# Kernel optimization log

Measured on AMD Instinct MI355X. Metric: run time of the kernel, lower is better.

The kernel has to match this reference:

```python
import jax, jax.numpy as jnp
import numpy as np
import math

N_NODES = 100000
N_EDGES = 1600000
IN_C, HID_C, OUT_C = 512, 128, 64
N_LAYERS = 8
ALPHA = 0.1
THETA = 0.5


def setup_inputs() -> dict:
    key = jax.random.key(0)
    ks = jax.random.split(key, 6)
    x = jax.random.normal(ks[0], (N_NODES, IN_C), dtype=jnp.float32)
    edge_index = jax.random.randint(ks[1], (2, N_EDGES), 0, N_NODES, dtype=jnp.int32)
    edge_weight = jax.random.uniform(ks[2], (N_EDGES,), dtype=jnp.float32)
    # parameters (scaled for numerical sanity)
    W_enc = jax.random.normal(ks[3], (HID_C, IN_C), dtype=jnp.float32) * (1.0 / math.sqrt(IN_C))
    W_convs = jax.random.normal(ks[4], (N_LAYERS, HID_C, HID_C), dtype=jnp.float32) * (1.0 / math.sqrt(HID_C))
    W_dec = jax.random.normal(ks[5], (OUT_C, HID_C), dtype=jnp.float32) * (1.0 / math.sqrt(HID_C))
    return {"x": x, "edge_index": edge_index, "edge_weight": edge_weight,
            "W_enc": W_enc, "W_convs": W_convs, "W_dec": W_dec}


def reference(x, edge_index, edge_weight, W_enc, W_convs, W_dec):
    # eval mode: dropout is a no-op
    src, dst = edge_index[0], edge_index[1]
    h = x @ W_enc.T                      # [N, HID]
    x0 = h                               # initial residual
    for i in range(N_LAYERS):
        # sparse neighbor aggregation: agg[d] = sum_e w_e * h[src_e]
        msg = h[src] * edge_weight[:, None]                      # [E, HID]
        agg = jax.ops.segment_sum(msg, dst, num_segments=N_NODES)
        hh = (1.0 - ALPHA) * agg + ALPHA * x0                    # initial residual
        beta = math.log(THETA / (i + 1) + 1.0)                   # identity mapping weight
        h = jax.nn.relu((1.0 - beta) * hh + beta * (hh @ W_convs[i]))
    return h @ W_dec.T                   # [N, OUT]
```

## Files before the change

kernel.cpp:

```cpp
#include <hip/hip_runtime.h>
#include <math.h>

#define N_NODES 100000
#define N_EDGES 1600000
#define IN_C 512
#define HID_C 128
#define OUT_C 64
#define N_LAYERS 8

typedef short bf16x8 __attribute__((ext_vector_type(8)));
typedef float f32x4 __attribute__((ext_vector_type(4)));

static __device__ __forceinline__ ushort f2bf(float f) {
  uint u = __float_as_uint(f);
  u = (u + 0x7FFFu + ((u >> 16) & 1u)) >> 16;
  return (ushort)u;
}
static __device__ __forceinline__ float bflo(uint u) { return __uint_as_float(u << 16); }
static __device__ __forceinline__ float bfhi(uint u) { return __uint_as_float(u & 0xffff0000u); }

__global__ __launch_bounds__(256) void hist_kernel(const int* __restrict__ dst,
                                                   int* __restrict__ cnt) {
  int e = blockIdx.x * 256 + threadIdx.x;
  atomicAdd(&cnt[dst[e]], 1);
}

__global__ __launch_bounds__(256) void scan_block(const int* __restrict__ in,
                                                  int* __restrict__ out,
                                                  int* __restrict__ bsum, int n) {
  __shared__ int tsum[256];
  int t = threadIdx.x;
  int base = blockIdx.x * 1024 + t * 4;
  int v0 = (base + 0 < n) ? in[base + 0] : 0;
  int v1 = (base + 1 < n) ? in[base + 1] : 0;
  int v2 = (base + 2 < n) ? in[base + 2] : 0;
  int v3 = (base + 3 < n) ? in[base + 3] : 0;
  int s = v0 + v1 + v2 + v3;
  tsum[t] = s;
  __syncthreads();
  for (int off = 1; off < 256; off <<= 1) {
    int x = (t >= off) ? tsum[t - off] : 0;
    __syncthreads();
    tsum[t] += x;
    __syncthreads();
  }
  int excl = tsum[t] - s;
  int i0 = excl + v0, i1 = i0 + v1, i2 = i1 + v2, i3 = i2 + v3;
  if (base + 0 < n) out[base + 0] = i0;
  if (base + 1 < n) out[base + 1] = i1;
  if (base + 2 < n) out[base + 2] = i2;
  if (base + 3 < n) out[base + 3] = i3;
  if (t == 255 && bsum) bsum[blockIdx.x] = tsum[255];
}

__global__ __launch_bounds__(256) void finalize_rows(const int* __restrict__ incl,
                                                     const int* __restrict__ auxi,
                                                     int* __restrict__ row, int n) {
  int i = blockIdx.x * 256 + threadIdx.x;
  if (i < n) {
    int g = i >> 10;
    int off = g ? auxi[g - 1] : 0;
    row[i + 1] = incl[i] + off;
    if (i == 0) row[0] = 0;
  }
}

__global__ __launch_bounds__(256) void init_cursor(const int* __restrict__ row,
                                                   int* __restrict__ cur, int n) {
  int i = blockIdx.x * 256 + threadIdx.x;
  if (i < n) cur[i] = row[i];
}

__global__ __launch_bounds__(256) void fill_csr(const int* __restrict__ src,
                                                const int* __restrict__ dst,
                                                const float* __restrict__ w,
                                                int* __restrict__ cur,
                                                uint* __restrict__ epk) {
  int e = blockIdx.x * 256 + threadIdx.x;
  int d = dst[e];
  int p = atomicAdd(&cur[d], 1);
  uint fb = __float_as_uint(w[e]) + 0x8000u;
  epk[p] = ((fb >> 16) << 17) | (uint)src[e];
}

__global__ __launch_bounds__(256) void cast_weights(const float* __restrict__ we,
                                                    const float* __restrict__ wc,
                                                    const float* __restrict__ wd,
                                                    ushort* __restrict__ web,
                                                    ushort* __restrict__ wcb,
                                                    ushort* __restrict__ wdb) {
  int i = blockIdx.x * 256 + threadIdx.x;
  if (i < 128 * 512) web[i] = f2bf(we[i]);
  if (i < 8 * 128 * 128) {
    int layer = i >> 14, rem = i & 16383, k = rem >> 7, j = rem & 127;
    wcb[(layer << 14) + (j << 7) + k] = f2bf(wc[i]);
  }
  if (i < 64 * 128) wdb[i] = f2bf(wd[i]);
}

__global__ __launch_bounds__(256) void enc_mfma(const float* __restrict__ x,
                                                const ushort* __restrict__ wb,
                                                ushort* __restrict__ h) {
  __shared__ ushort xs[32][136];
  __shared__ ushort ws[128][136];
  int tid = threadIdx.x;
  size_t row0 = (size_t)blockIdx.x * 32;
  int lane = tid & 63;
  int wv = tid >> 6;
  int m0 = (wv >> 1) * 16;
  int n0 = (wv & 1) * 64;
  int arow = m0 + (lane & 15);
  int akb = (lane >> 4) * 8;
  f32x4 acc[4] = {};
  for (int kc = 0; kc < 4; kc++) {
    int k0 = kc * 128;
    __syncthreads();
#pragma unroll
    for (int i = 0; i < 4; i++) {
      int u = tid + i * 256;
      int r = u >> 5, c4 = u & 31;
      float4 v = *(const float4*)(x + (row0 + r) * IN_C + k0 + c4 * 4);
      uint2 p;
      p.x = (uint)f2bf(v.x) | ((uint)f2bf(v.y) << 16);
      p.y = (uint)f2bf(v.z) | ((uint)f2bf(v.w) << 16);
      *(uint2*)&xs[r][c4 * 4] = p;
    }
#pragma unroll
    for (int i = 0; i < 8; i++) {
      int u = tid + i * 256;
      int c = u >> 4, o = u & 15;
      *(uint4*)&ws[c][o * 8] = *(const uint4*)(wb + (size_t)c * IN_C + k0 + o * 8);
    }
    __syncthreads();
#pragma unroll
    for (int ks = 0; ks < 4; ks++) {
      int kk = ks * 32 + akb;
      bf16x8 a = *(bf16x8*)&xs[arow][kk];
#pragma unroll
      for (int n = 0; n < 4; n++) {
        bf16x8 b = *(bf16x8*)&ws[n0 + n * 16 + (lane & 15)][kk];
        acc[n] = __builtin_amdgcn_mfma_f32_16x16x32_bf16(a, b, acc[n], 0, 0, 0);
      }
    }
  }
  int crow = m0 + (lane >> 4) * 4;
  int ccol = lane & 15;
#pragma unroll
  for (int n = 0; n < 4; n++)
#pragma unroll
    for (int r = 0; r < 4; r++)
      h[(row0 + crow + r) * HID_C + n0 + n * 16 + ccol] = f2bf(acc[n][r]);
}

__global__ __launch_bounds__(256) void agg_bf(const ushort* __restrict__ h,
                                              const ushort* __restrict__ x0,
                                              const int* __restrict__ row,
                                              const uint* __restrict__ epk,
                                              ushort* __restrict__ out) {
  int node = (blockIdx.x * 256 + threadIdx.x) >> 6;
  int lane = threadIdx.x & 63;
  int beg = row[node], end = row[node + 1];
  float a0 = 0.f, a1 = 0.f;
  const uint* hp = (const uint*)h + lane;
  for (int e = beg; e < end; e += 8) {
    uint p0 = (e + 0 < end) ? epk[e + 0] : 0u;
    uint p1 = (e + 1 < end) ? epk[e + 1] : 0u;
    uint p2 = (e + 2 < end) ? epk[e + 2] : 0u;
    uint p3 = (e + 3 < end) ? epk[e + 3] : 0u;
    uint p4 = (e + 4 < end) ? epk[e + 4] : 0u;
    uint p5 = (e + 5 < end) ? epk[e + 5] : 0u;
    uint p6 = (e + 6 < end) ? epk[e + 6] : 0u;
    uint p7 = (e + 7 < end) ? epk[e + 7] : 0u;
    uint h0 = hp[(size_t)(p0 & 0x1FFFFu) * 64];
    uint h1 = hp[(size_t)(p1 & 0x1FFFFu) * 64];
    uint h2 = hp[(size_t)(p2 & 0x1FFFFu) * 64];
    uint h3 = hp[(size_t)(p3 & 0x1FFFFu) * 64];
    uint h4 = hp[(size_t)(p4 & 0x1FFFFu) * 64];
    uint h5 = hp[(size_t)(p5 & 0x1FFFFu) * 64];
    uint h6 = hp[(size_t)(p6 & 0x1FFFFu) * 64];
    uint h7 = hp[(size_t)(p7 & 0x1FFFFu) * 64];
    float w0 = __uint_as_float((p0 >> 17) << 16);
    float w1 = __uint_as_float((p1 >> 17) << 16);
    float w2 = __uint_as_float((p2 >> 17) << 16);
    float w3 = __uint_as_float((p3 >> 17) << 16);
    float w4 = __uint_as_float((p4 >> 17) << 16);
    float w5 = __uint_as_float((p5 >> 17) << 16);
    float w6 = __uint_as_float((p6 >> 17) << 16);
    float w7 = __uint_as_float((p7 >> 17) << 16);
    a0 = fmaf(w0, bflo(h0), a0); a1 = fmaf(w0, bfhi(h0), a1);
    a0 = fmaf(w1, bflo(h1), a0); a1 = fmaf(w1, bfhi(h1), a1);
    a0 = fmaf(w2, bflo(h2), a0); a1 = fmaf(w2, bfhi(h2), a1);
    a0 = fmaf(w3, bflo(h3), a0); a1 = fmaf(w3, bfhi(h3), a1);
    a0 = fmaf(w4, bflo(h4), a0); a1 = fmaf(w4, bfhi(h4), a1);
    a0 = fmaf(w5, bflo(h5), a0); a1 = fmaf(w5, bfhi(h5), a1);
    a0 = fmaf(w6, bflo(h6), a0); a1 = fmaf(w6, bfhi(h6), a1);
    a0 = fmaf(w7, bflo(h7), a0); a1 = fmaf(w7, bfhi(h7), a1);
  }
  uint xv = ((const uint*)x0)[(size_t)node * 64 + lane];
  float o0 = 0.9f * a0 + 0.1f * bflo(xv);
  float o1 = 0.9f * a1 + 0.1f * bfhi(xv);
  ((uint*)out)[(size_t)node * 64 + lane] = (uint)f2bf(o0) | ((uint)f2bf(o1) << 16);
}

__global__ __launch_bounds__(256) void conv_mfma(ushort* __restrict__ hbuf,
                                                 const ushort* __restrict__ wb,
                                                 float onemb, float beta) {
  __shared__ ushort hs[32][136];
  __shared__ ushort ws[128][136];
  int tid = threadIdx.x;
  size_t row0 = (size_t)blockIdx.x * 32;
  {
    int r = tid >> 3, o = tid & 7;
    *(uint4*)&hs[r][o * 16] = *(const uint4*)(hbuf + (row0 + r) * HID_C + o * 16);
    *(uint4*)&hs[r][o * 16 + 8] = *(const uint4*)(hbuf + (row0 + r) * HID_C + o * 16 + 8);
  }
#pragma unroll
  for (int i = 0; i < 8; i++) {
    int u = tid + i * 256;
    int c = u >> 4, o = u & 15;
    *(uint4*)&ws[c][o * 8] = *(const uint4*)(wb + (size_t)c * HID_C + o * 8);
  }
  __syncthreads();
  int lane = tid & 63;
  int wv = tid >> 6;
  int m0 = (wv >> 1) * 16, n0 = (wv & 1) * 64;
  int arow = m0 + (lane & 15), akb = (lane >> 4) * 8;
  f32x4 acc[4] = {};
#pragma unroll
  for (int ks = 0; ks < 4; ks++) {
    int kk = ks * 32 + akb;
    bf16x8 a = *(bf16x8*)&hs[arow][kk];
#pragma unroll
    for (int n = 0; n < 4; n++) {
      bf16x8 b = *(bf16x8*)&ws[n0 + n * 16 + (lane & 15)][kk];
      acc[n] = __builtin_amdgcn_mfma_f32_16x16x32_bf16(a, b, acc[n], 0, 0, 0);
    }
  }
  __syncthreads();
  int crow = m0 + (lane >> 4) * 4, ccol = lane & 15;
#pragma unroll
  for (int n = 0; n < 4; n++)
#pragma unroll
    for (int r = 0; r < 4; r++) {
      float hv = bflo((uint)hs[crow + r][n0 + n * 16 + ccol]);
      float o = fmaxf(onemb * hv + beta * acc[n][r], 0.f);
      hbuf[(row0 + crow + r) * HID_C + n0 + n * 16 + ccol] = f2bf(o);
    }
}

__global__ __launch_bounds__(256) void dec_mfma(const ushort* __restrict__ h,
                                                const ushort* __restrict__ wb,
                                                float* __restrict__ out) {
  __shared__ ushort hs[32][136];
  __shared__ ushort ws[64][136];
  int tid = threadIdx.x;
  size_t row0 = (size_t)blockIdx.x * 32;
  {
    int r = tid >> 3, o = tid & 7;
    *(uint4*)&hs[r][o * 16] = *(const uint4*)(h + (row0 + r) * HID_C + o * 16);
    *(uint4*)&hs[r][o * 16 + 8] = *(const uint4*)(h + (row0 + r) * HID_C + o * 16 + 8);
  }
#pragma unroll
  for (int i = 0; i < 4; i++) {
    int u = tid + i * 256;
    int c = u >> 4, o = u & 15;
    *(uint4*)&ws[c][o * 8] = *(const uint4*)(wb + (size_t)c * HID_C + o * 8);
  }
  __syncthreads();
  int lane = tid & 63, wv = tid >> 6;
  int m0 = (wv >> 1) * 16, n0 = (wv & 1) * 32;
  int arow = m0 + (lane & 15), akb = (lane >> 4) * 8;
  f32x4 acc[2] = {};
#pragma unroll
  for (int ks = 0; ks < 4; ks++) {
    int kk = ks * 32 + akb;
    bf16x8 a = *(bf16x8*)&hs[arow][kk];
#pragma unroll
    for (int n = 0; n < 2; n++) {
      bf16x8 b = *(bf16x8*)&ws[n0 + n * 16 + (lane & 15)][kk];
      acc[n] = __builtin_amdgcn_mfma_f32_16x16x32_bf16(a, b, acc[n], 0, 0, 0);
    }
  }
  int crow = m0 + (lane >> 4) * 4, ccol = lane & 15;
#pragma unroll
  for (int n = 0; n < 2; n++)
#pragma unroll
    for (int r = 0; r < 4; r++)
      out[(row0 + crow + r) * OUT_C + n0 + n * 16 + ccol] = acc[n][r];
}

extern "C" void kernel_launch(void* const* d_in, const int* in_sizes, int n_in,
                              void* d_out, int out_size, void* d_ws, size_t ws_size,
                              hipStream_t stream) {
  const float* x = (const float*)d_in[0];
  const int* ei = (const int*)d_in[1];
  const float* ew = (const float*)d_in[2];
  const float* Wenc = (const float*)d_in[3];
  const float* Wconvs = (const float*)d_in[4];
  const float* Wdec = (const float*)d_in[5];
  float* out = (float*)d_out;

  char* p = (char*)d_ws;
  ushort* H0 = (ushort*)p; p += (size_t)N_NODES * HID_C * 2;
  ushort* HA = (ushort*)p; p += (size_t)N_NODES * HID_C * 2;
  ushort* HB = (ushort*)p; p += (size_t)N_NODES * HID_C * 2;
  uint* EPK = (uint*)p;    p += (size_t)N_EDGES * 4;
  ushort* WENC = (ushort*)p;  p += 128 * 512 * 2;
  ushort* WCONV = (ushort*)p; p += 8 * 128 * 128 * 2;
  ushort* WDEC = (ushort*)p;  p += 64 * 128 * 2;
  int* ROW = (int*)p;  p += (N_NODES + 1) * 4;
  int* CNT = (int*)p;  p += N_NODES * 4;
  int* INCL = (int*)p; p += N_NODES * 4;
  int* CUR = (int*)p;  p += N_NODES * 4;
  int* AUX = (int*)p;  p += 128 * 4;
  int* AUXI = (int*)p;

  const int* src = ei;
  const int* dst = ei + N_EDGES;

  cast_weights<<<512, 256, 0, stream>>>(Wenc, Wconvs, Wdec, WENC, WCONV, WDEC);

  hipMemsetAsync(CNT, 0, N_NODES * sizeof(int), stream);
  hist_kernel<<<N_EDGES / 256, 256, 0, stream>>>(dst, CNT);
  scan_block<<<98, 256, 0, stream>>>(CNT, INCL, AUX, N_NODES);
  scan_block<<<1, 256, 0, stream>>>(AUX, AUXI, nullptr, 98);
  finalize_rows<<<391, 256, 0, stream>>>(INCL, AUXI, ROW, N_NODES);
  init_cursor<<<391, 256, 0, stream>>>(ROW, CUR, N_NODES);
  fill_csr<<<N_EDGES / 256, 256, 0, stream>>>(src, dst, ew, CUR, EPK);

  enc_mfma<<<3125, 256, 0, stream>>>(x, WENC, H0);

  const ushort* cur = H0;
  ushort* bufs[2] = {HA, HB};
  for (int i = 0; i < N_LAYERS; i++) {
    ushort* nxt = bufs[i & 1];
    agg_bf<<<25000, 256, 0, stream>>>(cur, H0, ROW, EPK, nxt);
    float beta = logf(0.5f / (float)(i + 1) + 1.0f);
    conv_mfma<<<3125, 256, 0, stream>>>(nxt, WCONV + (size_t)i * HID_C * HID_C,
                                        1.0f - beta, beta);
    cur = nxt;
  }

  dec_mfma<<<3125, 256, 0, stream>>>(cur, WDEC, out);
}
```

Before: 835.1 us.

## Two-pass binned CSR build and 64-row conv tiles

Replaces the per-edge atomic scatter CSR fill with a two-pass scheme. Edges are first bucketed into 1024-node bins, using a block-local histogram and coalesced writes to a staging buffer. A per-bin kernel then places each edge using shared-memory atomic cursors. The goal is to cut random global atomics and scattered writes, at the cost of an extra 8-byte-per-edge staging buffer and another pass. The conv kernel also processes 64 rows per block with each wave covering all 128 columns, which halves the grid and removes the second barrier.

```diff
diff --git a/kernel.cpp b/kernel.cpp
--- a/kernel.cpp
+++ b/kernel.cpp
@@ -65,22 +65,88 @@
   }
 }
 
-__global__ __launch_bounds__(256) void init_cursor(const int* __restrict__ row,
-                                                   int* __restrict__ cur, int n) {
-  int i = blockIdx.x * 256 + threadIdx.x;
-  if (i < n) cur[i] = row[i];
-}
-
-__global__ __launch_bounds__(256) void fill_csr(const int* __restrict__ src,
-                                                const int* __restrict__ dst,
-                                                const float* __restrict__ w,
-                                                int* __restrict__ cur,
-                                                uint* __restrict__ epk) {
-  int e = blockIdx.x * 256 + threadIdx.x;
-  int d = dst[e];
-  int p = atomicAdd(&cur[d], 1);
-  uint fb = __float_as_uint(w[e]) + 0x8000u;
-  epk[p] = ((fb >> 16) << 17) | (uint)src[e];
+__global__ __launch_bounds__(128) void init_bincur(const int* __restrict__ row,
+                                                   int* __restrict__ bincur) {
+  int b = threadIdx.x;
+  int n0 = b << 10;
+  bincur[b] = row[n0 < N_NODES ? n0 : N_NODES];
+}
+
+__global__ __launch_bounds__(256) void bin_scatter(const int* __restrict__ src,
+                                                   const int* __restrict__ dst,
+                                                   const float* __restrict__ w,
+                                                   int* __restrict__ bincur,
+                                                   uint2* __restrict__ bb) {
+  __shared__ uint2 ebuf[2048];
+  __shared__ int hist[128];
+  __shared__ int lstart[128];
+  __shared__ int gbase[128];
+  int tid = threadIdx.x;
+  int base = blockIdx.x * 2048;
+  int cnt = N_EDGES - base;
+  if (cnt > 2048) cnt = 2048;
+  if (tid < 128) hist[tid] = 0;
+  __syncthreads();
+  uint pay[8];
+  int bn[8], rk[8], dfull[8];
+#pragma unroll
+  for (int i = 0; i < 8; i++) {
+    int idx = tid + i * 256;
+    if (idx < cnt) {
+      int e = base + idx;
+      int d = dst[e];
+      uint fb = __float_as_uint(w[e]) + 0x8000u;
+      pay[i] = ((fb >> 16) << 17) | (uint)src[e];
+      dfull[i] = d;
+      bn[i] = d >> 10;
+      rk[i] = atomicAdd(&hist[bn[i]], 1);
+    }
+  }
+  __syncthreads();
+  if (tid == 0) {
+    int acc = 0;
+    for (int b = 0; b < 128; b++) { lstart[b] = acc; acc += hist[b]; }
+  }
+  __syncthreads();
+  if (tid < 128 && hist[tid] > 0) gbase[tid] = atomicAdd(&bincur[tid], hist[tid]);
+  __syncthreads();
+#pragma unroll
+  for (int i = 0; i < 8; i++) {
+    int idx = tid + i * 256;
+    if (idx < cnt) ebuf[lstart[bn[i]] + rk[i]] = make_uint2(pay[i], (uint)dfull[i]);
+  }
+  __syncthreads();
+#pragma unroll
+  for (int i = 0; i < 8; i++) {
+    int j = tid + i * 256;
+    if (j < cnt) {
+      uint2 v = ebuf[j];
+      int b = (int)(v.y >> 10);
+      bb[gbase[b] + (j - lstart[b])] = v;
+    }
+  }
+}
+
+__global__ __launch_bounds__(256) void bin_place(const uint2* __restrict__ bb,
+                                                 const int* __restrict__ row,
+                                                 uint* __restrict__ epk) {
+  __shared__ int lcur[1024];
+  int b = blockIdx.x;
+  int n0 = b << 10;
+  int tid = threadIdx.x;
+  for (int i = tid; i < 1024; i += 256) {
+    int d = n0 + i;
+    lcur[i] = (d < N_NODES) ? row[d] : 0;
+  }
+  __syncthreads();
+  int hi = n0 + 1024;
+  if (hi > N_NODES) hi = N_NODES;
+  int beg = row[n0], end = row[hi];
+  for (int j = beg + tid; j < end; j += 256) {
+    uint2 v = bb[j];
+    int p = atomicAdd(&lcur[v.y & 1023u], 1);
+    epk[p] = v.x;
+  }
 }
 
 __global__ __launch_bounds__(256) void cast_weights(const float* __restrict__ we,
@@ -205,14 +271,16 @@
 __global__ __launch_bounds__(256) void conv_mfma(ushort* __restrict__ hbuf,
                                                  const ushort* __restrict__ wb,
                                                  float onemb, float beta) {
-  __shared__ ushort hs[32][136];
+  __shared__ ushort hs[64][136];
   __shared__ ushort ws[128][136];
   int tid = threadIdx.x;
-  size_t row0 = (size_t)blockIdx.x * 32;
-  {
-    int r = tid >> 3, o = tid & 7;
-    *(uint4*)&hs[r][o * 16] = *(const uint4*)(hbuf + (row0 + r) * HID_C + o * 16);
-    *(uint4*)&hs[r][o * 16 + 8] = *(const uint4*)(hbuf + (row0 + r) * HID_C + o * 16 + 8);
+  size_t row0 = (size_t)blockIdx.x * 64;
+#pragma unroll
+  for (int i = 0; i < 4; i++) {
+    int u = tid + i * 256;
+    int r = u >> 4, o = u & 15;
+    if (row0 + r < N_NODES)
+      *(uint4*)&hs[r][o * 8] = *(const uint4*)(hbuf + (row0 + r) * HID_C + o * 8);
   }
 #pragma unroll
   for (int i = 0; i < 8; i++) {
@@ -223,28 +291,29 @@
   __syncthreads();
   int lane = tid & 63;
   int wv = tid >> 6;
-  int m0 = (wv >> 1) * 16, n0 = (wv & 1) * 64;
+  int m0 = wv * 16;
   int arow = m0 + (lane & 15), akb = (lane >> 4) * 8;
-  f32x4 acc[4] = {};
+  f32x4 acc[8] = {};
 #pragma unroll
   for (int ks = 0; ks < 4; ks++) {
     int kk = ks * 32 + akb;
     bf16x8 a = *(bf16x8*)&hs[arow][kk];
 #pragma unroll
-    for (int n = 0; n < 4; n++) {
-      bf16x8 b = *(bf16x8*)&ws[n0 + n * 16 + (lane & 15)][kk];
+    for (int n = 0; n < 8; n++) {
+      bf16x8 b = *(bf16x8*)&ws[n * 16 + (lane & 15)][kk];
       acc[n] = __builtin_amdgcn_mfma_f32_16x16x32_bf16(a, b, acc[n], 0, 0, 0);
     }
   }
-  __syncthreads();
   int crow = m0 + (lane >> 4) * 4, ccol = lane & 15;
 #pragma unroll
-  for (int n = 0; n < 4; n++)
+  for (int n = 0; n < 8; n++)
 #pragma unroll
     for (int r = 0; r < 4; r++) {
-      float hv = bflo((uint)hs[crow + r][n0 + n * 16 + ccol]);
-      float o = fmaxf(onemb * hv + beta * acc[n][r], 0.f);
-      hbuf[(row0 + crow + r) * HID_C + n0 + n * 16 + ccol] = f2bf(o);
+      if (row0 + crow + r < N_NODES) {
+        float hv = bflo((uint)hs[crow + r][n * 16 + ccol]);
+        float o = fmaxf(onemb * hv + beta * acc[n][r], 0.f);
+        hbuf[(row0 + crow + r) * HID_C + n * 16 + ccol] = f2bf(o);
+      }
     }
 }
 
@@ -305,13 +374,14 @@
   ushort* HA = (ushort*)p; p += (size_t)N_NODES * HID_C * 2;
   ushort* HB = (ushort*)p; p += (size_t)N_NODES * HID_C * 2;
   uint* EPK = (uint*)p;    p += (size_t)N_EDGES * 4;
+  uint2* BB = (uint2*)p;   p += (size_t)N_EDGES * 8;
   ushort* WENC = (ushort*)p;  p += 128 * 512 * 2;
   ushort* WCONV = (ushort*)p; p += 8 * 128 * 128 * 2;
   ushort* WDEC = (ushort*)p;  p += 64 * 128 * 2;
   int* ROW = (int*)p;  p += (N_NODES + 1) * 4;
   int* CNT = (int*)p;  p += N_NODES * 4;
   int* INCL = (int*)p; p += N_NODES * 4;
-  int* CUR = (int*)p;  p += N_NODES * 4;
+  int* BINCUR = (int*)p; p += 128 * 4;
   int* AUX = (int*)p;  p += 128 * 4;
   int* AUXI = (int*)p;
 
@@ -325,8 +395,9 @@
   scan_block<<<98, 256, 0, stream>>>(CNT, INCL, AUX, N_NODES);
   scan_block<<<1, 256, 0, stream>>>(AUX, AUXI, nullptr, 98);
   finalize_rows<<<391, 256, 0, stream>>>(INCL, AUXI, ROW, N_NODES);
-  init_cursor<<<391, 256, 0, stream>>>(ROW, CUR, N_NODES);
-  fill_csr<<<N_EDGES / 256, 256, 0, stream>>>(src, dst, ew, CUR, EPK);
+  init_bincur<<<1, 128, 0, stream>>>(ROW, BINCUR);
+  bin_scatter<<<(N_EDGES + 2047) / 2048, 256, 0, stream>>>(src, dst, ew, BINCUR, BB);
+  bin_place<<<98, 256, 0, stream>>>(BB, ROW, EPK);
 
   enc_mfma<<<3125, 256, 0, stream>>>(x, WENC, H0);
 
@@ -336,7 +407,7 @@
     ushort* nxt = bufs[i & 1];
     agg_bf<<<25000, 256, 0, stream>>>(cur, H0, ROW, EPK, nxt);
     float beta = logf(0.5f / (float)(i + 1) + 1.0f);
-    conv_mfma<<<3125, 256, 0, stream>>>(nxt, WCONV + (size_t)i * HID_C * HID_C,
+    conv_mfma<<<1563, 256, 0, stream>>>(nxt, WCONV + (size_t)i * HID_C * HID_C,
                                         1.0f - beta, beta);
     cur = nxt;
   }
```

New measurement: 847.7 us. No clear change (+1.5%).
